# Kernel optimization log

Measured on AMD Instinct MI355X. Metric: run time of the kernel, lower is better.

## Reference

```python
import jax, jax.numpy as jnp
import numpy as np

B, C, H, W = 8, 64, 64, 64
CI = 32  # inter_channels = in_channels // 2
EPS = 1e-5


def conv1x1(x, w, b=None):
    # x: (b,c,h,w), w: (o,c) -> (b,o,h,w)
    y = jnp.einsum('bchw,oc->bohw', x, w)
    if b is not None:
        y = y + b[None, :, None, None]
    return y


def maxpool2x2(x):
    b, c, h, w = x.shape
    return x.reshape(b, c, h // 2, 2, w // 2, 2).max(axis=(3, 5))


def setup_inputs() -> dict:
    key = jax.random.key(0)
    ks = jax.random.split(key, 12)
    s = 0.05
    return {
        'x': jax.random.normal(ks[0], (B, C, H, W), jnp.float32),
        'theta_w': jax.random.normal(ks[1], (CI, C), jnp.float32) * s,
        'theta_b': jax.random.normal(ks[2], (CI,), jnp.float32) * s,
        'phi_w': jax.random.normal(ks[3], (CI, C), jnp.float32) * s,
        'phi_b': jax.random.normal(ks[4], (CI,), jnp.float32) * s,
        'psi_w': jax.random.normal(ks[5], (CI, C), jnp.float32) * s,
        'psi_b': jax.random.normal(ks[6], (CI,), jnp.float32) * s,
        'cp_w': jax.random.normal(ks[7], (2 * CI,), jnp.float32) * s,  # concat_project 1x1, no bias
        'W_w': jax.random.normal(ks[8], (C, CI + 1), jnp.float32) * s,
        'W_b': jax.random.normal(ks[9], (C,), jnp.float32) * s,
        'bn_gamma': jax.random.normal(ks[10], (C,), jnp.float32) * s + 1.0,
        'bn_beta': jax.random.normal(ks[11], (C,), jnp.float32) * s,
    }


def reference(x, theta_w, theta_b, phi_w, phi_b, psi_w, psi_b, cp_w, W_w, W_b, bn_gamma, bn_beta):
    b = x.shape[0]
    # psi / phi branches get 2x2 maxpool (sub_sample=True default)
    psi_x = maxpool2x2(conv1x1(x, psi_w, psi_b)).reshape(b, CI, -1)      # (b,ci,M)
    psi_x = psi_x.transpose(0, 2, 1)                                     # (b,M,ci)
    theta_x = conv1x1(x, theta_w, theta_b).reshape(b, CI, -1)            # (b,ci,N)
    phi_x = maxpool2x2(conv1x1(x, phi_w, phi_b)).reshape(b, CI, -1)      # (b,ci,M)
    # concat_project(cat[theta_i, phi_j]) + ReLU == relu(w1.theta_i + w2.phi_j)
    w1, w2 = cp_w[:CI], cp_w[CI:]
    a = jnp.einsum('bcn,c->bn', theta_x, w1)                             # (b,N)
    bb = jnp.einsum('bcm,c->bm', phi_x, w2)                              # (b,M)
    f = jax.nn.relu(a[:, :, None] + bb[:, None, :])                      # (b,N,M)
    M = f.shape[-1]
    f_div_C = f / float(M)
    y = jnp.matmul(f_div_C, psi_x)                                       # (b,N,ci)
    y = y.transpose(0, 2, 1).reshape(b, CI, H, W)
    # r_structure_type='zero' -> zero structure channel
    structure_feat = jnp.zeros((b, 1, H, W), y.dtype)
    y = jnp.concatenate([y, structure_feat], axis=1)                     # (b,ci+1,H,W)
    wy = conv1x1(y, W_w, W_b)                                            # (b,C,H,W)
    # BatchNorm2d, training-mode batch stats, biased variance
    mu = wy.mean(axis=(0, 2, 3), keepdims=True)
    var = wy.var(axis=(0, 2, 3), keepdims=True)
    wy = (wy - mu) * jax.lax.rsqrt(var + EPS)
    wy = wy * bn_gamma[None, :, None, None] + bn_beta[None, :, None, None]
    return wy + x
```

## Files before the change

kernel.cpp:

```cpp
#include <hip/hip_runtime.h>

#define OFF_A    0
#define OFF_BB   32768
#define OFF_SBB  40960
#define OFF_PERM 49152
#define OFF_U    57344
#define OFF_T1   581632
#define OFF_T2   1106432
#define OFF_KK   1631232
#define OFF_M    1664000
#define OFF_HC   1664128
#define OFF_HS   1672328
#define OFF_HS2  1680528

__global__ __launch_bounds__(256) void kA(
    const float* __restrict__ x, const float* __restrict__ theta_w,
    const float* __restrict__ theta_b, const float* __restrict__ phi_w,
    const float* __restrict__ phi_b, const float* __restrict__ psi_w,
    const float* __restrict__ psi_b, const float* __restrict__ cp_w,
    const float* __restrict__ Ww, float* ws)
{
    __shared__ float sm[4160];
    __shared__ float spsi[8*33];
    __shared__ float sWw[64*33];
    int tid = threadIdx.x;
    int bid = blockIdx.x;
    if (bid < 1024) {
        for (int e = tid; e < 2048; e += 256) {
            int i = e >> 6, c = e & 63;
            sm[i*130 + 2*c]     = phi_w[e];
            sm[i*130 + 2*c + 1] = psi_w[e];
        }
        for (int e = tid; e < 2048; e += 256)
            sWw[(e >> 5)*33 + (e & 31)] = Ww[(e >> 5)*33 + (e & 31)];
        __syncthreads();
        int t = (bid << 8) + tid;
        int i = t & 31;
        int m = (t >> 5) & 1023;
        int b = t >> 15;
        int ph = m >> 5, pw = m & 31;
        const float* xb = x + b*262144 + ph*128 + pw*2;
        const float2* wrow = (const float2*)(sm + i*130);
        float p0=0,p1=0,p2=0,p3=0,s0=0,s1=0,s2=0,s3=0;
        #pragma unroll 8
        for (int c = 0; c < 64; ++c) {
            float2 xa = *(const float2*)(xb + c*4096);
            float2 xc = *(const float2*)(xb + c*4096 + 64);
            float2 w  = wrow[c];
            p0 += xa.x*w.x; p1 += xa.y*w.x; p2 += xc.x*w.x; p3 += xc.y*w.x;
            s0 += xa.x*w.y; s1 += xa.y*w.y; s2 += xc.x*w.y; s3 += xc.y*w.y;
        }
        float pv = fmaxf(fmaxf(p0,p1), fmaxf(p2,p3)) + phi_b[i];
        float sv = fmaxf(fmaxf(s0,s1), fmaxf(s2,s3)) + psi_b[i];
        spsi[(tid >> 5)*33 + i] = sv;
        float v = pv * cp_w[32 + i];
        v += __shfl_xor(v, 16, 32);
        v += __shfl_xor(v,  8, 32);
        v += __shfl_xor(v,  4, 32);
        v += __shfl_xor(v,  2, 32);
        v += __shfl_xor(v,  1, 32);
        if (i == 0) ws[OFF_BB + (b<<10) + m] = v;
        __syncthreads();
        int m0 = (bid & 127) << 3;
        #pragma unroll
        for (int rep = 0; rep < 2; ++rep) {
            int idx = tid + (rep << 8);
            int ml = idx >> 6, o = idx & 63;
            const float* pr = &spsi[ml*33];
            const float* wr = &sWw[o*33];
            float u = 0;
            #pragma unroll
            for (int i2 = 0; i2 < 32; ++i2) u += pr[i2]*wr[i2];
            ws[OFF_U + (((b<<10) + m0 + ml) << 6) + o] = u;
        }
    } else {
        if (bid == 1024) {
            for (int e = tid; e < 24728; e += 256) ws[OFF_M + e] = 0.0f;
        }
        if (tid < 64) {
            float s = 0;
            for (int i = 0; i < 32; ++i) s += cp_w[i]*theta_w[i*64 + tid];
            sm[tid] = s;
        } else if (tid == 64) {
            float s = 0;
            for (int i = 0; i < 32; ++i) s += cp_w[i]*theta_b[i];
            sm[64] = s;
        }
        __syncthreads();
        int t = ((bid - 1024) << 8) + tid;
        int n = t & 4095, b = t >> 12;
        const float* xb = x + b*262144 + n;
        float acc = sm[64];
        #pragma unroll 8
        for (int c = 0; c < 64; ++c) acc += xb[c*4096]*sm[c];
        ws[OFF_A + t] = acc;
    }
}

__global__ __launch_bounds__(256) void kRank(float* ws)
{
    __shared__ float sb[1024];
    int tid = threadIdx.x;
    int b = blockIdx.x >> 5, chunk = blockIdx.x & 31;
    const float* bb = ws + OFF_BB + (b<<10);
    for (int e = tid; e < 1024; e += 256) sb[e] = bb[e];
    __syncthreads();
    {
        int ml = tid >> 3, jl = tid & 7;
        int m = (chunk<<5) + ml;
        float v = sb[m];
        int cnt = 0;
        for (int s = 0; s < 128; ++s) {
            int j = jl + (s<<3);
            float u = sb[j];
            cnt += (u > v || (u == v && j < m)) ? 1 : 0;
        }
        cnt += __shfl_xor(cnt, 1, 8);
        cnt += __shfl_xor(cnt, 2, 8);
        cnt += __shfl_xor(cnt, 4, 8);
        if (jl == 0) {
            ws[OFF_SBB + (b<<10) + cnt] = v;
            ((int*)ws)[OFF_PERM + (b<<10) + cnt] = m;
        }
    }
    {
        int l = tid >> 1, jl = tid & 1;
        int n = (chunk<<7) + l;
        float av = ws[OFF_A + (b<<12) + n];
        float tt = -av;
        const float2* sb2 = (const float2*)sb;
        int cnt = 0;
        for (int s = 0; s < 256; ++s) {
            float2 u = sb2[jl + (s<<1)];
            cnt += (u.x > tt) ? 1 : 0;
            cnt += (u.y > tt) ? 1 : 0;
        }
        cnt += __shfl_xor(cnt, 1, 64);
        if (jl == 0) {
            ((int*)ws)[OFF_KK + (b<<12) + n] = cnt;
            atomicAdd(&ws[OFF_HC + b*1025 + cnt], 1.0f);
            atomicAdd(&ws[OFF_HS + b*1025 + cnt], av);
            atomicAdd(&ws[OFF_HS2 + b*1025 + cnt], av*av);
        }
    }
}

__global__ __launch_bounds__(1024) void kPS(float* ws)
{
    __shared__ float ssort[1024];
    __shared__ int   sperm[1024];
    __shared__ float shc[1025], shs[1025], shs2[1025];
    __shared__ float swp1[128], swp2[128];
    int tid = threadIdx.x;
    int b = blockIdx.x >> 3, og = blockIdx.x & 7;
    int obase = og << 3;
    ssort[tid] = ws[OFF_SBB + (b<<10) + tid];
    sperm[tid] = ((const int*)ws)[OFF_PERM + (b<<10) + tid];
    shc[tid]  = ws[OFF_HC  + b*1025 + tid];
    shs[tid]  = ws[OFF_HS  + b*1025 + tid];
    shs2[tid] = ws[OFF_HS2 + b*1025 + tid];
    if (tid == 0) {
        shc[1024]  = ws[OFF_HC  + b*1025 + 1024];
        shs[1024]  = ws[OFF_HS  + b*1025 + 1024];
        shs2[1024] = ws[OFF_HS2 + b*1025 + 1024];
    }
    __syncthreads();
    int ch = tid >> 3, o = tid & 7;
    int wv = tid >> 6, chl = (tid & 63) >> 3;
    const float* Ub = ws + OFF_U + (b<<16) + obase + o;
    float p[8], sp[8];
    float s1 = 0, s2 = 0;
    #pragma unroll
    for (int jl = 0; jl < 8; ++jl) {
        int jj = (ch<<3) + jl;
        float v = Ub[sperm[jj]<<6];
        p[jl] = v;
        sp[jl] = ssort[jj]*v;
        s1 += v; s2 += sp[jl];
    }
    float own1 = s1, own2 = s2;
    #pragma unroll
    for (int d = 1; d < 8; d <<= 1) {
        float u1 = __shfl_up(s1, d<<3, 64);
        float u2 = __shfl_up(s2, d<<3, 64);
        if (chl >= d) { s1 += u1; s2 += u2; }
    }
    if (chl == 7) { swp1[(wv<<3)+o] = s1; swp2[(wv<<3)+o] = s2; }
    __syncthreads();
    float off1 = 0, off2 = 0;
    for (int w = 0; w < 16; ++w) {
        if (w < wv) { off1 += swp1[(w<<3)+o]; off2 += swp2[(w<<3)+o]; }
    }
    float run1 = off1 + s1 - own1;
    float run2 = off2 + s2 - own2;
    float* T1 = ws + OFF_T1 + b*65600 + obase + o;
    float* T2 = ws + OFF_T2 + b*65600 + obase + o;
    if (ch == 0) { T1[0] = 0.0f; T2[0] = 0.0f; }
    const float inv = 1.0f/1024.0f;
    float m1 = 0, m2 = 0;
    #pragma unroll
    for (int jl = 0; jl < 8; ++jl) {
        int k = (ch<<3) + jl + 1;
        run1 += p[jl]; run2 += sp[jl];
        float t1 = run1*inv, t2 = run2*inv;
        T1[k<<6] = t1;
        T2[k<<6] = t2;
        float c = shc[k], sa = shs[k], sa2 = shs2[k];
        m1 += sa*t1 + c*t2;
        m2 += (sa2*t1 + 2.0f*sa*t2)*t1 + c*t2*t2;
    }
    m1 += __shfl_xor(m1,  8, 64); m2 += __shfl_xor(m2,  8, 64);
    m1 += __shfl_xor(m1, 16, 64); m2 += __shfl_xor(m2, 16, 64);
    m1 += __shfl_xor(m1, 32, 64); m2 += __shfl_xor(m2, 32, 64);
    __syncthreads();
    if (chl == 0) { swp1[(wv<<3)+o] = m1; swp2[(wv<<3)+o] = m2; }
    __syncthreads();
    if (tid < 8) {
        float a1 = 0, a2 = 0;
        for (int w = 0; w < 16; ++w) { a1 += swp1[(w<<3)+tid]; a2 += swp2[(w<<3)+tid]; }
        atomicAdd(&ws[OFF_M + obase + tid], a1);
        atomicAdd(&ws[OFF_M + 64 + obase + tid], a2);
    }
}

__global__ __launch_bounds__(256) void kFinal(
    const float* __restrict__ x, const float* __restrict__ Wb,
    const float* __restrict__ gamma, const float* __restrict__ beta,
    const float* __restrict__ ws, float* __restrict__ out)
{
    __shared__ float tile[64*65];
    __shared__ float sa[64];
    __shared__ int   sk[64];
    __shared__ float sA[64];
    __shared__ float sD[64];
    int tid = threadIdx.x;
    int b = blockIdx.x >> 6;
    int n0 = (blockIdx.x & 63) << 6;
    if (tid < 64) {
        sa[tid] = ws[OFF_A + (b<<12) + n0 + tid];
        sk[tid] = ((const int*)ws)[OFF_KK + (b<<12) + n0 + tid];
        const float Ninv = 1.0f/32768.0f;
        float m1 = ws[OFF_M + tid] * Ninv;
        float m2 = ws[OFF_M + 64 + tid] * Ninv;
        float wb = Wb[tid];
        float mu  = m1 + wb;
        float E2  = m2 + 2.0f*wb*m1 + wb*wb;
        float var = E2 - mu*mu;
        float A = gamma[tid] * rsqrtf(var + 1e-5f);
        sA[tid] = A;
        sD[tid] = beta[tid] + A*(wb - mu);
    }
    __syncthreads();
    const float* T1 = ws + OFF_T1 + b*65600;
    const float* T2 = ws + OFF_T2 + b*65600;
    {
        int o = tid & 63, ng = tid >> 6;
        float Ao = sA[o], Do = sD[o];
        for (int j = 0; j < 16; ++j) {
            int n = (ng << 4) + j;
            int k = sk[n];
            float a = sa[n];
            float t1 = T1[(k<<6) + o];
            float t2 = T2[(k<<6) + o];
            tile[o*65 + n] = Ao*(a*t1 + t2) + Do;
        }
    }
    __syncthreads();
    {
        int n = tid & 63, og = tid >> 6;
        for (int j = 0; j < 16; ++j) {
            int o = (og << 4) + j;
            int idx = ((b<<6) + o)*4096 + n0 + n;
            out[idx] = tile[o*65 + n] + x[idx];
        }
    }
}

extern "C" void kernel_launch(void* const* d_in, const int* in_sizes, int n_in,
                              void* d_out, int out_size, void* d_ws, size_t ws_size,
                              hipStream_t stream)
{
    const float* x       = (const float*)d_in[0];
    const float* theta_w = (const float*)d_in[1];
    const float* theta_b = (const float*)d_in[2];
    const float* phi_w   = (const float*)d_in[3];
    const float* phi_b   = (const float*)d_in[4];
    const float* psi_w   = (const float*)d_in[5];
    const float* psi_b   = (const float*)d_in[6];
    const float* cp_w    = (const float*)d_in[7];
    const float* Ww      = (const float*)d_in[8];
    const float* Wb      = (const float*)d_in[9];
    const float* gamma   = (const float*)d_in[10];
    const float* beta    = (const float*)d_in[11];
    float* ws  = (float*)d_ws;
    float* out = (float*)d_out;

    kA<<<1152, 256, 0, stream>>>(x, theta_w, theta_b, phi_w, phi_b,
                                 psi_w, psi_b, cp_w, Ww, ws);
    kRank<<<256, 256, 0, stream>>>(ws);
    kPS<<<64, 1024, 0, stream>>>(ws);
    kFinal<<<512, 256, 0, stream>>>(x, Wb, gamma, beta, ws, out);
}
```

Before: 130.8 us.

## Fuse four kernels into one cooperative persistent kernel with grid syncs

Replaces the four launches with a single cooperative kernel of 256 blocks of 1024 threads, separated by grid.sync barriers. The theta projection is folded into the phi/psi pooling loop, so x is read once for both. The rank and final stages are re-tiled for the larger blocks. The aim is to remove kernel launch gaps and redundant x reads, at the cost of grid-barrier overhead, only 256 blocks in flight, and stage 3 leaving most blocks idle.

```diff
diff --git a/kernel.cpp b/kernel.cpp
--- a/kernel.cpp
+++ b/kernel.cpp
@@ -1,4 +1,7 @@
 #include <hip/hip_runtime.h>
+#include <hip/hip_cooperative_groups.h>
+
+namespace cg = cooperative_groups;
 
 #define OFF_A    0
 #define OFF_BB   32768
@@ -13,265 +16,277 @@
 #define OFF_HS   1672328
 #define OFF_HS2  1680528
 
-__global__ __launch_bounds__(256) void kA(
+__global__ __launch_bounds__(1024) void kMega(
     const float* __restrict__ x, const float* __restrict__ theta_w,
     const float* __restrict__ theta_b, const float* __restrict__ phi_w,
     const float* __restrict__ phi_b, const float* __restrict__ psi_w,
     const float* __restrict__ psi_b, const float* __restrict__ cp_w,
-    const float* __restrict__ Ww, float* ws)
+    const float* __restrict__ Ww, const float* __restrict__ Wb,
+    const float* __restrict__ gamma, const float* __restrict__ beta,
+    float* __restrict__ ws, float* __restrict__ out)
 {
-    __shared__ float sm[4160];
-    __shared__ float spsi[8*33];
-    __shared__ float sWw[64*33];
-    int tid = threadIdx.x;
-    int bid = blockIdx.x;
-    if (bid < 1024) {
-        for (int e = tid; e < 2048; e += 256) {
+    __shared__ float sh[8640];
+    cg::grid_group grid = cg::this_grid();
+    const int tid = threadIdx.x;
+    const int bid = blockIdx.x;
+    const int b   = bid >> 5;
+    const int sub = bid & 31;
+
+    {
+        float* sm   = sh;
+        float* sth  = sh + 4160;
+        float* spsi = sh + 4228;
+        float* sWw  = sh + 5284;
+        for (int e = tid; e < 2048; e += 1024) {
             int i = e >> 6, c = e & 63;
             sm[i*130 + 2*c]     = phi_w[e];
             sm[i*130 + 2*c + 1] = psi_w[e];
         }
-        for (int e = tid; e < 2048; e += 256)
+        for (int e = tid; e < 2048; e += 1024)
             sWw[(e >> 5)*33 + (e & 31)] = Ww[(e >> 5)*33 + (e & 31)];
-        __syncthreads();
-        int t = (bid << 8) + tid;
-        int i = t & 31;
-        int m = (t >> 5) & 1023;
-        int b = t >> 15;
+        if (tid < 64) {
+            float s = 0;
+            for (int i = 0; i < 32; ++i) s += cp_w[i]*theta_w[i*64 + tid];
+            sth[tid] = s;
+        } else if (tid == 64) {
+            float s = 0;
+            for (int i = 0; i < 32; ++i) s += cp_w[i]*theta_b[i];
+            sth[64] = s;
+        }
+        if (bid == 0) {
+            for (int e = tid; e < 24728; e += 1024) ws[OFF_M + e] = 0.0f;
+        }
+        __syncthreads();
+        int i = tid & 31;
+        int mIdx = tid >> 5;
+        int m = (sub << 5) + mIdx;
         int ph = m >> 5, pw = m & 31;
         const float* xb = x + b*262144 + ph*128 + pw*2;
         const float2* wrow = (const float2*)(sm + i*130);
+        float tb = sth[64];
         float p0=0,p1=0,p2=0,p3=0,s0=0,s1=0,s2=0,s3=0;
+        float a0=tb,a1=tb,a2=tb,a3=tb;
         #pragma unroll 8
         for (int c = 0; c < 64; ++c) {
             float2 xa = *(const float2*)(xb + c*4096);
             float2 xc = *(const float2*)(xb + c*4096 + 64);
             float2 w  = wrow[c];
+            float st  = sth[c];
             p0 += xa.x*w.x; p1 += xa.y*w.x; p2 += xc.x*w.x; p3 += xc.y*w.x;
             s0 += xa.x*w.y; s1 += xa.y*w.y; s2 += xc.x*w.y; s3 += xc.y*w.y;
+            a0 += xa.x*st;  a1 += xa.y*st;  a2 += xc.x*st;  a3 += xc.y*st;
         }
         float pv = fmaxf(fmaxf(p0,p1), fmaxf(p2,p3)) + phi_b[i];
         float sv = fmaxf(fmaxf(s0,s1), fmaxf(s2,s3)) + psi_b[i];
-        spsi[(tid >> 5)*33 + i] = sv;
+        spsi[mIdx*33 + i] = sv;
         float v = pv * cp_w[32 + i];
         v += __shfl_xor(v, 16, 32);
         v += __shfl_xor(v,  8, 32);
         v += __shfl_xor(v,  4, 32);
         v += __shfl_xor(v,  2, 32);
         v += __shfl_xor(v,  1, 32);
-        if (i == 0) ws[OFF_BB + (b<<10) + m] = v;
-        __syncthreads();
-        int m0 = (bid & 127) << 3;
+        if (i == 0) {
+            ws[OFF_BB + (b<<10) + m] = v;
+            int nb = (b<<12) + ph*128 + pw*2;
+            ws[OFF_A + nb]      = a0;
+            ws[OFF_A + nb + 1]  = a1;
+            ws[OFF_A + nb + 64] = a2;
+            ws[OFF_A + nb + 65] = a3;
+        }
+        __syncthreads();
         #pragma unroll
         for (int rep = 0; rep < 2; ++rep) {
-            int idx = tid + (rep << 8);
+            int idx = tid + (rep << 10);
             int ml = idx >> 6, o = idx & 63;
             const float* pr = &spsi[ml*33];
             const float* wr = &sWw[o*33];
             float u = 0;
             #pragma unroll
             for (int i2 = 0; i2 < 32; ++i2) u += pr[i2]*wr[i2];
-            ws[OFF_U + (((b<<10) + m0 + ml) << 6) + o] = u;
-        }
-    } else {
-        if (bid == 1024) {
-            for (int e = tid; e < 24728; e += 256) ws[OFF_M + e] = 0.0f;
+            ws[OFF_U + (((b<<10) + (sub<<5) + ml) << 6) + o] = u;
+        }
+    }
+    grid.sync();
+
+    {
+        float* sb = sh;
+        sb[tid] = ws[OFF_BB + (b<<10) + tid];
+        __syncthreads();
+        {
+            int ml = tid >> 5, jl = tid & 31;
+            int m = (sub << 5) + ml;
+            float vv = sb[m];
+            int cnt = 0;
+            for (int s = 0; s < 32; ++s) {
+                int j = jl + (s << 5);
+                float u = sb[j];
+                cnt += (u > vv || (u == vv && j < m)) ? 1 : 0;
+            }
+            cnt += __shfl_xor(cnt,  1, 32);
+            cnt += __shfl_xor(cnt,  2, 32);
+            cnt += __shfl_xor(cnt,  4, 32);
+            cnt += __shfl_xor(cnt,  8, 32);
+            cnt += __shfl_xor(cnt, 16, 32);
+            if (jl == 0) {
+                ws[OFF_SBB + (b<<10) + cnt] = vv;
+                ((int*)ws)[OFF_PERM + (b<<10) + cnt] = m;
+            }
+        }
+        {
+            int l = tid >> 3, jl = tid & 7;
+            int n = (sub << 7) + l;
+            float av = ws[OFF_A + (b<<12) + n];
+            float tt = -av;
+            const float2* sb2 = (const float2*)sb;
+            int cnt = 0;
+            for (int s = 0; s < 64; ++s) {
+                float2 u = sb2[jl + (s << 3)];
+                cnt += (u.x > tt) ? 1 : 0;
+                cnt += (u.y > tt) ? 1 : 0;
+            }
+            cnt += __shfl_xor(cnt, 1, 8);
+            cnt += __shfl_xor(cnt, 2, 8);
+            cnt += __shfl_xor(cnt, 4, 8);
+            if (jl == 0) {
+                ((int*)ws)[OFF_KK + (b<<12) + n] = cnt;
+                atomicAdd(&ws[OFF_HC + b*1025 + cnt], 1.0f);
+                atomicAdd(&ws[OFF_HS + b*1025 + cnt], av);
+                atomicAdd(&ws[OFF_HS2 + b*1025 + cnt], av*av);
+            }
+        }
+    }
+    grid.sync();
+
+    if (bid < 64) {
+        int b3 = bid >> 3, og = bid & 7;
+        int obase = og << 3;
+        float* ssort = sh;
+        int*   sperm = (int*)(sh + 1024);
+        float* shc   = sh + 2048;
+        float* shs   = sh + 3076;
+        float* shs2  = sh + 4104;
+        float* swp1  = sh + 5132;
+        float* swp2  = sh + 5260;
+        ssort[tid] = ws[OFF_SBB + (b3<<10) + tid];
+        sperm[tid] = ((const int*)ws)[OFF_PERM + (b3<<10) + tid];
+        shc[tid]  = ws[OFF_HC  + b3*1025 + tid];
+        shs[tid]  = ws[OFF_HS  + b3*1025 + tid];
+        shs2[tid] = ws[OFF_HS2 + b3*1025 + tid];
+        if (tid == 0) {
+            shc[1024]  = ws[OFF_HC  + b3*1025 + 1024];
+            shs[1024]  = ws[OFF_HS  + b3*1025 + 1024];
+            shs2[1024] = ws[OFF_HS2 + b3*1025 + 1024];
+        }
+        __syncthreads();
+        int ch = tid >> 3, o = tid & 7;
+        int wv = tid >> 6, chl = (tid & 63) >> 3;
+        const float* Ub = ws + OFF_U + (b3<<16) + obase + o;
+        float p[8], sp[8];
+        float s1 = 0, s2 = 0;
+        #pragma unroll
+        for (int jl = 0; jl < 8; ++jl) {
+            int jj = (ch<<3) + jl;
+            float v = Ub[sperm[jj]<<6];
+            p[jl] = v;
+            sp[jl] = ssort[jj]*v;
+            s1 += v; s2 += sp[jl];
+        }
+        float own1 = s1, own2 = s2;
+        #pragma unroll
+        for (int d = 1; d < 8; d <<= 1) {
+            float u1 = __shfl_up(s1, d<<3, 64);
+            float u2 = __shfl_up(s2, d<<3, 64);
+            if (chl >= d) { s1 += u1; s2 += u2; }
+        }
+        if (chl == 7) { swp1[(wv<<3)+o] = s1; swp2[(wv<<3)+o] = s2; }
+        __syncthreads();
+        float off1 = 0, off2 = 0;
+        for (int w = 0; w < 16; ++w) {
+            if (w < wv) { off1 += swp1[(w<<3)+o]; off2 += swp2[(w<<3)+o]; }
+        }
+        float run1 = off1 + s1 - own1;
+        float run2 = off2 + s2 - own2;
+        float* T1 = ws + OFF_T1 + b3*65600 + obase + o;
+        float* T2 = ws + OFF_T2 + b3*65600 + obase + o;
+        if (ch == 0) { T1[0] = 0.0f; T2[0] = 0.0f; }
+        const float inv = 1.0f/1024.0f;
+        float m1 = 0, m2 = 0;
+        #pragma unroll
+        for (int jl = 0; jl < 8; ++jl) {
+            int k = (ch<<3) + jl + 1;
+            run1 += p[jl]; run2 += sp[jl];
+            float t1 = run1*inv, t2 = run2*inv;
+            T1[k<<6] = t1;
+            T2[k<<6] = t2;
+            float c = shc[k], sa_ = shs[k], sa2 = shs2[k];
+            m1 += sa_*t1 + c*t2;
+            m2 += (sa2*t1 + 2.0f*sa_*t2)*t1 + c*t2*t2;
+        }
+        m1 += __shfl_xor(m1,  8, 64); m2 += __shfl_xor(m2,  8, 64);
+        m1 += __shfl_xor(m1, 16, 64); m2 += __shfl_xor(m2, 16, 64);
+        m1 += __shfl_xor(m1, 32, 64); m2 += __shfl_xor(m2, 32, 64);
+        __syncthreads();
+        if (chl == 0) { swp1[(wv<<3)+o] = m1; swp2[(wv<<3)+o] = m2; }
+        __syncthreads();
+        if (tid < 8) {
+            float a1 = 0, a2 = 0;
+            for (int w = 0; w < 16; ++w) {
+                a1 += swp1[(w<<3)+tid]; a2 += swp2[(w<<3)+tid];
+            }
+            atomicAdd(&ws[OFF_M + obase + tid], a1);
+            atomicAdd(&ws[OFF_M + 64 + obase + tid], a2);
+        }
+    }
+    grid.sync();
+
+    {
+        float* tile = sh;
+        float* sa = sh + 8256;
+        int*   sk = (int*)(sh + 8384);
+        float* sA = sh + 8512;
+        float* sD = sh + 8576;
+        int n0 = sub << 7;
+        if (tid < 128) {
+            sa[tid] = ws[OFF_A + (b<<12) + n0 + tid];
+            sk[tid] = ((const int*)ws)[OFF_KK + (b<<12) + n0 + tid];
         }
         if (tid < 64) {
-            float s = 0;
-            for (int i = 0; i < 32; ++i) s += cp_w[i]*theta_w[i*64 + tid];
-            sm[tid] = s;
-        } else if (tid == 64) {
-            float s = 0;
-            for (int i = 0; i < 32; ++i) s += cp_w[i]*theta_b[i];
-            sm[64] = s;
-        }
-        __syncthreads();
-        int t = ((bid - 1024) << 8) + tid;
-        int n = t & 4095, b = t >> 12;
-        const float* xb = x + b*262144 + n;
-        float acc = sm[64];
-        #pragma unroll 8
-        for (int c = 0; c < 64; ++c) acc += xb[c*4096]*sm[c];
-        ws[OFF_A + t] = acc;
-    }
-}
-
-__global__ __launch_bounds__(256) void kRank(float* ws)
-{
-    __shared__ float sb[1024];
-    int tid = threadIdx.x;
-    int b = blockIdx.x >> 5, chunk = blockIdx.x & 31;
-    const float* bb = ws + OFF_BB + (b<<10);
-    for (int e = tid; e < 1024; e += 256) sb[e] = bb[e];
-    __syncthreads();
-    {
-        int ml = tid >> 3, jl = tid & 7;
-        int m = (chunk<<5) + ml;
-        float v = sb[m];
-        int cnt = 0;
-        for (int s = 0; s < 128; ++s) {
-            int j = jl + (s<<3);
-            float u = sb[j];
-            cnt += (u > v || (u == v && j < m)) ? 1 : 0;
-        }
-        cnt += __shfl_xor(cnt, 1, 8);
-        cnt += __shfl_xor(cnt, 2, 8);
-        cnt += __shfl_xor(cnt, 4, 8);
-        if (jl == 0) {
-            ws[OFF_SBB + (b<<10) + cnt] = v;
-            ((int*)ws)[OFF_PERM + (b<<10) + cnt] = m;
-        }
-    }
-    {
-        int l = tid >> 1, jl = tid & 1;
-        int n = (chunk<<7) + l;
-        float av = ws[OFF_A + (b<<12) + n];
-        float tt = -av;
-        const float2* sb2 = (const float2*)sb;
-        int cnt = 0;
-        for (int s = 0; s < 256; ++s) {
-            float2 u = sb2[jl + (s<<1)];
-            cnt += (u.x > tt) ? 1 : 0;
-            cnt += (u.y > tt) ? 1 : 0;
-        }
-        cnt += __shfl_xor(cnt, 1, 64);
-        if (jl == 0) {
-            ((int*)ws)[OFF_KK + (b<<12) + n] = cnt;
-            atomicAdd(&ws[OFF_HC + b*1025 + cnt], 1.0f);
-            atomicAdd(&ws[OFF_HS + b*1025 + cnt], av);
-            atomicAdd(&ws[OFF_HS2 + b*1025 + cnt], av*av);
-        }
-    }
-}
-
-__global__ __launch_bounds__(1024) void kPS(float* ws)
-{
-    __shared__ float ssort[1024];
-    __shared__ int   sperm[1024];
-    __shared__ float shc[1025], shs[1025], shs2[1025];
-    __shared__ float swp1[128], swp2[128];
-    int tid = threadIdx.x;
-    int b = blockIdx.x >> 3, og = blockIdx.x & 7;
-    int obase = og << 3;
-    ssort[tid] = ws[OFF_SBB + (b<<10) + tid];
-    sperm[tid] = ((const int*)ws)[OFF_PERM + (b<<10) + tid];
-    shc[tid]  = ws[OFF_HC  + b*1025 + tid];
-    shs[tid]  = ws[OFF_HS  + b*1025 + tid];
-    shs2[tid] = ws[OFF_HS2 + b*1025 + tid];
-    if (tid == 0) {
-        shc[1024]  = ws[OFF_HC  + b*1025 + 1024];
-        shs[1024]  = ws[OFF_HS  + b*1025 + 1024];
-        shs2[1024] = ws[OFF_HS2 + b*1025 + 1024];
-    }
-    __syncthreads();
-    int ch = tid >> 3, o = tid & 7;
-    int wv = tid >> 6, chl = (tid & 63) >> 3;
-    const float* Ub = ws + OFF_U + (b<<16) + obase + o;
-    float p[8], sp[8];
-    float s1 = 0, s2 = 0;
-    #pragma unroll
-    for (int jl = 0; jl < 8; ++jl) {
-        int jj = (ch<<3) + jl;
-        float v = Ub[sperm[jj]<<6];
-        p[jl] = v;
-        sp[jl] = ssort[jj]*v;
-        s1 += v; s2 += sp[jl];
-    }
-    float own1 = s1, own2 = s2;
-    #pragma unroll
-    for (int d = 1; d < 8; d <<= 1) {
-        float u1 = __shfl_up(s1, d<<3, 64);
-        float u2 = __shfl_up(s2, d<<3, 64);
-        if (chl >= d) { s1 += u1; s2 += u2; }
-    }
-    if (chl == 7) { swp1[(wv<<3)+o] = s1; swp2[(wv<<3)+o] = s2; }
-    __syncthreads();
-    float off1 = 0, off2 = 0;
-    for (int w = 0; w < 16; ++w) {
-        if (w < wv) { off1 += swp1[(w<<3)+o]; off2 += swp2[(w<<3)+o]; }
-    }
-    float run1 = off1 + s1 - own1;
-    float run2 = off2 + s2 - own2;
-    float* T1 = ws + OFF_T1 + b*65600 + obase + o;
-    float* T2 = ws + OFF_T2 + b*65600 + obase + o;
-    if (ch == 0) { T1[0] = 0.0f; T2[0] = 0.0f; }
-    const float inv = 1.0f/1024.0f;
-    float m1 = 0, m2 = 0;
-    #pragma unroll
-    for (int jl = 0; jl < 8; ++jl) {
-        int k = (ch<<3) + jl + 1;
-        run1 += p[jl]; run2 += sp[jl];
-        float t1 = run1*inv, t2 = run2*inv;
-        T1[k<<6] = t1;
-        T2[k<<6] = t2;
-        float c = shc[k], sa = shs[k], sa2 = shs2[k];
-        m1 += sa*t1 + c*t2;
-        m2 += (sa2*t1 + 2.0f*sa*t2)*t1 + c*t2*t2;
-    }
-    m1 += __shfl_xor(m1,  8, 64); m2 += __shfl_xor(m2,  8, 64);
-    m1 += __shfl_xor(m1, 16, 64); m2 += __shfl_xor(m2, 16, 64);
-    m1 += __shfl_xor(m1, 32, 64); m2 += __shfl_xor(m2, 32, 64);
-    __syncthreads();
-    if (chl == 0) { swp1[(wv<<3)+o] = m1; swp2[(wv<<3)+o] = m2; }
-    __syncthreads();
-    if (tid < 8) {
-        float a1 = 0, a2 = 0;
-        for (int w = 0; w < 16; ++w) { a1 += swp1[(w<<3)+tid]; a2 += swp2[(w<<3)+tid]; }
-        atomicAdd(&ws[OFF_M + obase + tid], a1);
-        atomicAdd(&ws[OFF_M + 64 + obase + tid], a2);
-    }
-}
-
-__global__ __launch_bounds__(256) void kFinal(
-    const float* __restrict__ x, const float* __restrict__ Wb,
-    const float* __restrict__ gamma, const float* __restrict__ beta,
-    const float* __restrict__ ws, float* __restrict__ out)
-{
-    __shared__ float tile[64*65];
-    __shared__ float sa[64];
-    __shared__ int   sk[64];
-    __shared__ float sA[64];
-    __shared__ float sD[64];
-    int tid = threadIdx.x;
-    int b = blockIdx.x >> 6;
-    int n0 = (blockIdx.x & 63) << 6;
-    if (tid < 64) {
-        sa[tid] = ws[OFF_A + (b<<12) + n0 + tid];
-        sk[tid] = ((const int*)ws)[OFF_KK + (b<<12) + n0 + tid];
-        const float Ninv = 1.0f/32768.0f;
-        float m1 = ws[OFF_M + tid] * Ninv;
-        float m2 = ws[OFF_M + 64 + tid] * Ninv;
-        float wb = Wb[tid];
-        float mu  = m1 + wb;
-        float E2  = m2 + 2.0f*wb*m1 + wb*wb;
-        float var = E2 - mu*mu;
-        float A = gamma[tid] * rsqrtf(var + 1e-5f);
-        sA[tid] = A;
-        sD[tid] = beta[tid] + A*(wb - mu);
-    }
-    __syncthreads();
-    const float* T1 = ws + OFF_T1 + b*65600;
-    const float* T2 = ws + OFF_T2 + b*65600;
-    {
-        int o = tid & 63, ng = tid >> 6;
-        float Ao = sA[o], Do = sD[o];
-        for (int j = 0; j < 16; ++j) {
-            int n = (ng << 4) + j;
-            int k = sk[n];
-            float a = sa[n];
-            float t1 = T1[(k<<6) + o];
-            float t2 = T2[(k<<6) + o];
-            tile[o*65 + n] = Ao*(a*t1 + t2) + Do;
-        }
-    }
-    __syncthreads();
-    {
-        int n = tid & 63, og = tid >> 6;
-        for (int j = 0; j < 16; ++j) {
-            int o = (og << 4) + j;
-            int idx = ((b<<6) + o)*4096 + n0 + n;
-            out[idx] = tile[o*65 + n] + x[idx];
+            const float Ninv = 1.0f/32768.0f;
+            float m1 = ws[OFF_M + tid] * Ninv;
+            float m2 = ws[OFF_M + 64 + tid] * Ninv;
+            float wb = Wb[tid];
+            float mu  = m1 + wb;
+            float E2  = m2 + 2.0f*wb*m1 + wb*wb;
+            float var = E2 - mu*mu;
+            float A = gamma[tid] * rsqrtf(var + 1e-5f);
+            sA[tid] = A;
+            sD[tid] = beta[tid] + A*(wb - mu);
+        }
+        __syncthreads();
+        const float* T1 = ws + OFF_T1 + b*65600;
+        const float* T2 = ws + OFF_T2 + b*65600;
+        {
+            int o = tid & 63, ng = tid >> 6;
+            float Ao = sA[o], Do = sD[o];
+            #pragma unroll
+            for (int j = 0; j < 8; ++j) {
+                int n = (ng << 3) + j;
+                int k = sk[n];
+                float a = sa[n];
+                float t1 = T1[(k<<6) + o];
+                float t2 = T2[(k<<6) + o];
+                tile[o*129 + n] = Ao*(a*t1 + t2) + Do;
+            }
+        }
+        __syncthreads();
+        {
+            int n = tid & 127, og = tid >> 7;
+            #pragma unroll
+            for (int j = 0; j < 8; ++j) {
+                int o = (og << 3) + j;
+                int idx = ((b<<6) + o)*4096 + n0 + n;
+                out[idx] = tile[o*129 + n] + x[idx];
+            }
         }
     }
 }
@@ -295,9 +310,10 @@
     float* ws  = (float*)d_ws;
     float* out = (float*)d_out;
 
-    kA<<<1152, 256, 0, stream>>>(x, theta_w, theta_b, phi_w, phi_b,
-                                 psi_w, psi_b, cp_w, Ww, ws);
-    kRank<<<256, 256, 0, stream>>>(ws);
-    kPS<<<64, 1024, 0, stream>>>(ws);
-    kFinal<<<512, 256, 0, stream>>>(x, Wb, gamma, beta, ws, out);
+    void* args[] = { (void*)&x, (void*)&theta_w, (void*)&theta_b,
+                     (void*)&phi_w, (void*)&phi_b, (void*)&psi_w,
+                     (void*)&psi_b, (void*)&cp_w, (void*)&Ww, (void*)&Wb,
+                     (void*)&gamma, (void*)&beta, (void*)&ws, (void*)&out };
+    hipLaunchCooperativeKernel((const void*)kMega, dim3(256), dim3(1024),
+                               args, 0, stream);
 }
```

New measurement: 224.5 us. 1.72x slower.
